# Optimization experiments

Measured on AMD Instinct MI355X. Metric: run time of the kernel, lower is better.

Reference implementation:

```python
import jax, jax.numpy as jnp
import numpy as np

KERNEL_SIZE = 16
STRIDE = 8
NEG = -1.0e9


def setup_inputs() -> dict:
    key = jax.random.key(0)
    k1, k2, k3, k4, k5 = jax.random.split(key, 5)
    B, C, L = 8, 512, 4096
    x = jax.random.normal(k1, (B, C, L), dtype=jnp.float32)
    mask = jax.random.randint(k2, (B, L), 0, 2).astype(bool)
    W = jax.random.normal(k3, (C, C), dtype=jnp.float32) * 0.02
    b = jax.random.normal(k4, (C,), dtype=jnp.float32) * 0.02
    v = jax.random.normal(k5, (C,), dtype=jnp.float32) * 0.02
    return {"x": x, "mask": mask, "W": W, "b": b, "v": v}


def reference(x, mask, W, b, v):
    # x: [B, C, L], mask: [B, L] (True = masked out)
    B, C, L = x.shape
    win, step = KERNEL_SIZE, STRIDE
    L_pool = 1 + (L - win) // step
    # per-token projection (identical across windows since proj is per-token)
    h = jnp.tanh(jnp.einsum('bcl,dc->bld', x, W) + b)      # [B, L, C]
    s = jnp.einsum('bld,d->bl', h, v)                       # [B, L]
    idx = jnp.arange(L_pool)[:, None] * step + jnp.arange(win)[None, :]
    sw = s[:, idx]
    mw = mask[:, idx]
    sw = jnp.where(mw, NEG, sw)
    w = jax.nn.softmax(sw, axis=-1)
    w = jnp.where(mw, 0.0, w)
    norm = jnp.clip(jnp.sum(w, axis=-1, keepdims=True), 1e-6, None)
    w = w / norm
    xw = x[:, :, idx]
    return jnp.einsum('bcpw,bpw->bcp', xw, w)               # [B, C, L_pool]
```

## Files before the change

kernel.cpp:

```cpp
#include <hip/hip_runtime.h>
#include <hip/hip_bf16.h>
#include <cmath>

#define Bsz 8
#define Csz 512
#define Lsz 4096
#define LPOOL 511
#define NEGV -1000000000.0f

typedef __attribute__((ext_vector_type(8))) short short8;
typedef __attribute__((ext_vector_type(4))) float float4v;

__device__ __forceinline__ float bf2f(short u) {
  unsigned int x = ((unsigned int)(unsigned short)u) << 16;
  return __builtin_bit_cast(float, x);
}

__device__ __forceinline__ float ftanh(float x) {
  float e = __expf(2.0f * x);
  return 1.0f - 2.0f * __builtin_amdgcn_rcpf(e + 1.0f);
}

__device__ __forceinline__ void gl_lds16(const __hip_bfloat16* g, void* l) {
  __builtin_amdgcn_global_load_lds(
      (const __attribute__((address_space(1))) unsigned int*)g,
      (__attribute__((address_space(3))) unsigned int*)l, 16, 0, 0);
}

__global__ __launch_bounds__(256) void prep(const unsigned char* __restrict__ mb,
    int* __restrict__ flag, const float* __restrict__ W,
    __hip_bfloat16* __restrict__ Wts) {
  const int tid = threadIdx.x;
  const int pb = blockIdx.x;
  if (pb == 0) {
    __shared__ int sf;
    if (tid == 0) sf = 0;
    __syncthreads();
    int f = 0;
    for (int i = tid; i < 4096; i += 256)
      if ((i & 3) && mb[i]) f = 1;
    if (f) atomicOr(&sf, 1);
    __syncthreads();
    if (tid == 0) *flag = sf;
  } else {
    int tg = (pb - 1) * 256 + tid;
    int d = tg >> 6, cg = tg & 63;
    float4 w0 = *(const float4*)(W + (size_t)d * 512 + cg * 8);
    float4 w1 = *(const float4*)(W + (size_t)d * 512 + cg * 8 + 4);
    __hip_bfloat16 hb[8];
    hb[0] = __float2bfloat16(w0.x); hb[1] = __float2bfloat16(w0.y);
    hb[2] = __float2bfloat16(w0.z); hb[3] = __float2bfloat16(w0.w);
    hb[4] = __float2bfloat16(w1.x); hb[5] = __float2bfloat16(w1.y);
    hb[6] = __float2bfloat16(w1.z); hb[7] = __float2bfloat16(w1.w);
    int nt = d >> 7, row = d & 127, ks = cg >> 2, seg = cg & 3;
    *(short8*)(Wts + (((size_t)nt * 16 + ks) * 512 + seg * 128 + row) * 8) = *(short8*)hb;
  }
}

__global__ __launch_bounds__(512, 2) void gemm_fused(
    const float* __restrict__ x, const __hip_bfloat16* __restrict__ Wts,
    const float* __restrict__ bias, const float* __restrict__ v,
    float* __restrict__ s, __hip_bfloat16* __restrict__ xbf) {
  __shared__ short8 sA[8192];
  __shared__ __align__(16) char sPool[17408];

  const int tid = threadIdx.x;
  const int lane = tid & 63, wave = tid >> 6;
  const int mt = blockIdx.x;
  const int b = mt >> 5;
  const int l0 = (mt & 31) << 7;

  {
    float* sXw = (float*)sPool + wave * 544;
    const int r = lane >> 1;
    const int q = lane & 1;
    const size_t rowbase =
        (((size_t)(b * Csz + r)) << 12) + (size_t)(l0 + wave * 16 + q * 8);
    const float* xg = x + rowbase;
    const int ll = lane & 15, kseg = lane >> 4;

    float4 a0 = *(const float4*)(xg);
    float4 a1 = *(const float4*)(xg + 4);
    float4 b0 = *(const float4*)(xg + (1u << 17));
    float4 b1 = *(const float4*)(xg + (1u << 17) + 4);
    float4 c0 = a0, c1 = a1;

    for (int cc = 0; cc < 16; ++cc) {
      if (cc < 14) {
        const float* xn = xg + ((size_t)(cc + 2) << 17);
        c0 = *(const float4*)(xn);
        c1 = *(const float4*)(xn + 4);
      }
      __hip_bfloat16 hb[8];
      hb[0] = __float2bfloat16(a0.x); hb[1] = __float2bfloat16(a0.y);
      hb[2] = __float2bfloat16(a0.z); hb[3] = __float2bfloat16(a0.w);
      hb[4] = __float2bfloat16(a1.x); hb[5] = __float2bfloat16(a1.y);
      hb[6] = __float2bfloat16(a1.z); hb[7] = __float2bfloat16(a1.w);
      *(short8*)(xbf + rowbase + ((size_t)cc << 17)) = *(short8*)hb;
      *(float4*)(&sXw[r * 17 + q * 8])     = a0;
      *(float4*)(&sXw[r * 17 + q * 8 + 4]) = a1;
      asm volatile("s_waitcnt lgkmcnt(0)" ::: "memory");
      __builtin_amdgcn_sched_barrier(0);
      float tv[8];
      #pragma unroll
      for (int j = 0; j < 8; ++j) tv[j] = sXw[(kseg * 8 + j) * 17 + ll];
      __hip_bfloat16 ab[8];
      #pragma unroll
      for (int j = 0; j < 8; ++j) ab[j] = __float2bfloat16(tv[j]);
      sA[(cc * 4 + kseg) * 128 + wave * 16 + ll] = *(short8*)ab;
      asm volatile("s_waitcnt lgkmcnt(0)" ::: "memory");
      __builtin_amdgcn_sched_barrier(0);
      a0 = b0; a1 = b1; b0 = c0; b1 = c1;
    }
  }

  const int lr = lane & 15, quad = lane >> 4;
  float bl[4][8], vl[4][8];
  #pragma unroll
  for (int nt = 0; nt < 4; ++nt)
    #pragma unroll
    for (int nf = 0; nf < 8; ++nf) {
      int n = nt * 128 + nf * 16 + lr;
      bl[nt][nf] = bias[n];
      vl[nt][nf] = v[n];
    }

  __syncthreads();
  short8 (*sB)[512] = (short8 (*)[512])sPool;
  gl_lds16(Wts + (size_t)(wave * 64 + lane) * 8, &sB[0][wave * 64]);
  __syncthreads();

  float4v acc[8];
  float sp[4];
  #pragma unroll
  for (int nf = 0; nf < 8; ++nf) acc[nf] = (float4v)0.f;
  #pragma unroll
  for (int reg = 0; reg < 4; ++reg) sp[reg] = 0.f;

  #pragma unroll
  for (int nt = 0; nt < 4; ++nt) {
    #pragma unroll 2
    for (int ks = 0; ks < 16; ++ks) {
      const int idx = nt * 16 + ks;
      const int cur = idx & 1;
      if (idx < 63) {
        const __hip_bfloat16* gb =
            Wts + ((size_t)(idx + 1) << 12) + (size_t)(wave * 64 + lane) * 8;
        gl_lds16(gb, &sB[cur ^ 1][wave * 64]);
        asm volatile("s_waitcnt vmcnt(1)" ::: "memory");
      } else {
        asm volatile("s_waitcnt vmcnt(0)" ::: "memory");
      }
      __builtin_amdgcn_sched_barrier(0);
      __builtin_amdgcn_s_barrier();
      short8 af = sA[(ks * 4 + quad) * 128 + wave * 16 + lr];
      short8 bfr[8];
      #pragma unroll
      for (int nf = 0; nf < 8; ++nf)
        bfr[nf] = sB[cur][quad * 128 + nf * 16 + lr];
      #pragma unroll
      for (int nf = 0; nf < 8; ++nf)
        acc[nf] = __builtin_amdgcn_mfma_f32_16x16x32_bf16(af, bfr[nf], acc[nf], 0, 0, 0);
      __builtin_amdgcn_s_barrier();
    }
    #pragma unroll
    for (int reg = 0; reg < 4; ++reg) {
      float pp = 0.f;
      #pragma unroll
      for (int nf = 0; nf < 8; ++nf)
        pp += ftanh(acc[nf][reg] + bl[nt][nf]) * vl[nt][nf];
      sp[reg] += pp;
    }
    #pragma unroll
    for (int nf = 0; nf < 8; ++nf) acc[nf] = (float4v)0.f;
  }

  #pragma unroll
  for (int reg = 0; reg < 4; ++reg) {
    float pv = sp[reg];
    pv += __shfl_xor(pv, 1, 16);
    pv += __shfl_xor(pv, 2, 16);
    pv += __shfl_xor(pv, 4, 16);
    pv += __shfl_xor(pv, 8, 16);
    if (lr == 0)
      s[mt * 128 + wave * 16 + quad * 4 + reg] = pv;
  }
}

__global__ __launch_bounds__(256) void pool2(const __hip_bfloat16* __restrict__ xbf,
    const float* __restrict__ s, const void* __restrict__ mask,
    const int* __restrict__ flag, float* __restrict__ out) {
  __shared__ float wl[8][17];
  const int t = threadIdx.x;
  const int p0 = blockIdx.x * 8, b = blockIdx.y;
  if (t < 8 && p0 + t < LPOOL) {
    const int p = p0 + t;
    const bool u8 = (*flag != 0);
    const unsigned char* m8 = (const unsigned char*)mask;
    const int* m32 = (const int*)mask;
    const int base = b * Lsz + p * 8;
    float sv[16]; int mv[16];
    float mx = -3.4e38f;
    #pragma unroll
    for (int w = 0; w < 16; ++w) {
      int mk = u8 ? (int)m8[base + w] : m32[base + w];
      float val = mk ? NEGV : s[base + w];
      sv[w] = val; mv[w] = mk;
      mx = fmaxf(mx, val);
    }
    float sum = 0.f;
    #pragma unroll
    for (int w = 0; w < 16; ++w) { sv[w] = expf(sv[w] - mx); sum += sv[w]; }
    float inv = 1.0f / sum;
    float norm = 0.f;
    #pragma unroll
    for (int w = 0; w < 16; ++w) { sv[w] = mv[w] ? 0.f : sv[w] * inv; norm += sv[w]; }
    norm = fmaxf(norm, 1e-6f);
    float rn = 1.0f / norm;
    #pragma unroll
    for (int w = 0; w < 16; ++w) wl[t][w] = sv[w] * rn;
  }
  __syncthreads();
  const int ci = t >> 3, pi = t & 7;
  const int p = p0 + pi;
  if (p >= LPOOL) return;
  float wr[16];
  #pragma unroll
  for (int w = 0; w < 16; ++w) wr[w] = wl[pi][w];
  #pragma unroll 4
  for (int it = 0; it < 16; ++it) {
    int c = it * 32 + ci;
    const __hip_bfloat16* xp = xbf + ((size_t)b * Csz + c) * Lsz + 8 * p;
    short8 lo = *(const short8*)xp;
    short8 hi = *(const short8*)(xp + 8);
    float acc = 0.f;
    #pragma unroll
    for (int j = 0; j < 8; ++j)
      acc += bf2f(lo[j]) * wr[j] + bf2f(hi[j]) * wr[8 + j];
    out[((size_t)b * Csz + c) * LPOOL + p] = acc;
  }
}

__global__ void detect_mask(const unsigned char* __restrict__ mb, int* __restrict__ flag) {
  __shared__ int sf;
  int t = threadIdx.x;
  if (t == 0) sf = 0;
  __syncthreads();
  int f = 0;
  for (int i = t; i < 4096; i += 256)
    if ((i & 3) && mb[i]) f = 1;
  if (f) atomicOr(&sf, 1);
  __syncthreads();
  if (t == 0) *flag = sf;
}

__global__ __launch_bounds__(256) void gemm_s_f32(const float* __restrict__ x,
    const float* __restrict__ W, const float* __restrict__ bias,
    const float* __restrict__ v, float* __restrict__ s_out) {
  __shared__ float sA[32][64];
  __shared__ float sB[32][68];
  __shared__ float s_acc[64];
  const int tid = threadIdx.x;
  const int b = blockIdx.y;
  const int l0 = blockIdx.x * 64;
  if (tid < 64) s_acc[tid] = 0.0f;
  const int tx = tid & 15;
  const int ty = tid >> 4;
  const float* xb = x + ((size_t)b * Csz) * Lsz + l0;
  for (int d0 = 0; d0 < Csz; d0 += 64) {
    float acc[4][4] = {{0.f}};
    for (int c0 = 0; c0 < Csz; c0 += 32) {
      __syncthreads();
      #pragma unroll
      for (int it = 0; it < 8; ++it) {
        int idx = tid + it * 256;
        int kc = idx >> 6, ml = idx & 63;
        sA[kc][ml] = xb[(size_t)(c0 + kc) * Lsz + ml];
      }
      #pragma unroll
      for (int it = 0; it < 8; ++it) {
        int idx = tid + it * 256;
        int kc = idx & 31, dj = idx >> 5;
        sB[kc][dj] = W[(size_t)(d0 + dj) * Csz + c0 + kc];
      }
      __syncthreads();
      #pragma unroll
      for (int kc = 0; kc < 32; ++kc) {
        float4 a  = *(const float4*)(&sA[kc][tx << 2]);
        float4 w4 = *(const float4*)(&sB[kc][ty << 2]);
        acc[0][0] += a.x * w4.x; acc[0][1] += a.x * w4.y; acc[0][2] += a.x * w4.z; acc[0][3] += a.x * w4.w;
        acc[1][0] += a.y * w4.x; acc[1][1] += a.y * w4.y; acc[1][2] += a.y * w4.z; acc[1][3] += a.y * w4.w;
        acc[2][0] += a.z * w4.x; acc[2][1] += a.z * w4.y; acc[2][2] += a.z * w4.z; acc[2][3] += a.z * w4.w;
        acc[3][0] += a.w * w4.x; acc[3][1] += a.w * w4.y; acc[3][2] += a.w * w4.z; acc[3][3] += a.w * w4.w;
      }
    }
    float part[4] = {0.f, 0.f, 0.f, 0.f};
    #pragma unroll
    for (int j = 0; j < 4; ++j) {
      int d = d0 + (ty << 2) + j;
      float bj = bias[d], vj = v[d];
      #pragma unroll
      for (int i = 0; i < 4; ++i)
        part[i] += tanhf(acc[i][j] + bj) * vj;
    }
    #pragma unroll
    for (int i = 0; i < 4; ++i)
      atomicAdd(&s_acc[(tx << 2) + i], part[i]);
  }
  __syncthreads();
  if (tid < 64) s_out[(size_t)b * Lsz + l0 + tid] = s_acc[tid];
}

__global__ void win_weights(const float* __restrict__ s, const void* __restrict__ mask,
                            const int* __restrict__ flag, float* __restrict__ wgt) {
  int t = blockIdx.x * blockDim.x + threadIdx.x;
  if (t >= Bsz * LPOOL) return;
  int b = t / LPOOL, p = t - b * LPOOL;
  const bool u8 = (*flag != 0);
  const unsigned char* m8 = (const unsigned char*)mask;
  const int* m32 = (const int*)mask;
  float sv[16]; int mv[16];
  float mx = -3.4e38f;
  int base = b * Lsz + p * 8;
  #pragma unroll
  for (int w = 0; w < 16; ++w) {
    int mk = u8 ? (int)m8[base + w] : m32[base + w];
    float val = mk ? NEGV : s[base + w];
    sv[w] = val; mv[w] = mk;
    mx = fmaxf(mx, val);
  }
  float sum = 0.f;
  #pragma unroll
  for (int w = 0; w < 16; ++w) { sv[w] = expf(sv[w] - mx); sum += sv[w]; }
  float inv = 1.0f / sum;
  float norm = 0.f;
  #pragma unroll
  for (int w = 0; w < 16; ++w) { sv[w] = mv[w] ? 0.f : sv[w] * inv; norm += sv[w]; }
  norm = fmaxf(norm, 1e-6f);
  float rn = 1.0f / norm;
  #pragma unroll
  for (int w = 0; w < 16; ++w) wgt[t * 16 + w] = sv[w] * rn;
}

__global__ __launch_bounds__(256) void pool_out(const float* __restrict__ x,
    const float* __restrict__ wgt, float* __restrict__ out) {
  __shared__ float xrow[Lsz];
  int bc = blockIdx.x;
  int c = bc & (Csz - 1);
  int b = bc >> 9;
  const float* xr = x + ((size_t)b * Csz + c) * Lsz;
  int tid = threadIdx.x;
  #pragma unroll
  for (int it = 0; it < 4; ++it) {
    int idx = (tid + it * 256) << 2;
    *(float4*)(&xrow[idx]) = *(const float4*)(&xr[idx]);
  }
  __syncthreads();
  const float* wb = wgt + (size_t)b * LPOOL * 16;
  float* ob = out + ((size_t)b * Csz + c) * LPOOL;
  for (int p = tid; p < LPOOL; p += 256) {
    const float4* wp = (const float4*)(wb + p * 16);
    const float4* xp = (const float4*)(&xrow[p * 8]);
    float acc = 0.f;
    #pragma unroll
    for (int q = 0; q < 4; ++q) {
      float4 wv = wp[q], xv = xp[q];
      acc += xv.x * wv.x + xv.y * wv.y + xv.z * wv.z + xv.w * wv.w;
    }
    ob[p] = acc;
  }
}

extern "C" void kernel_launch(void* const* d_in, const int* in_sizes, int n_in,
                              void* d_out, int out_size, void* d_ws, size_t ws_size,
                              hipStream_t stream) {
  const float* x    = (const float*)d_in[0];
  const void*  mask = d_in[1];
  const float* W    = (const float*)d_in[2];
  const float* bias = (const float*)d_in[3];
  const float* v    = (const float*)d_in[4];
  float* out = (float*)d_out;

  char* wsb = (char*)d_ws;
  int*   flag = (int*)wsb;
  float* s    = (float*)(wsb + 256);
  float* wgt  = (float*)(wsb + 131328);
  __hip_bfloat16* Wts = (__hip_bfloat16*)(wsb + 393216);
  __hip_bfloat16* xbf = (__hip_bfloat16*)(wsb + 917504);
  const size_t NEED = 917504 + 33554432;

  if (ws_size >= NEED) {
    prep<<<129, 256, 0, stream>>>((const unsigned char*)mask, flag, W, Wts);
    gemm_fused<<<256, 512, 0, stream>>>(x, Wts, bias, v, s, xbf);
    pool2<<<dim3(64, Bsz), 256, 0, stream>>>(xbf, s, mask, flag, out);
  } else {
    detect_mask<<<1, 256, 0, stream>>>((const unsigned char*)mask, flag);
    gemm_s_f32<<<dim3(Lsz / 64, Bsz), 256, 0, stream>>>(x, W, bias, v, s);
    win_weights<<<(Bsz * LPOOL + 255) / 256, 256, 0, stream>>>(s, mask, flag, wgt);
    pool_out<<<Bsz * Csz, 256, 0, stream>>>(x, wgt, out);
  }
}
```

Before: 163.9 us.

## Use single-wave GEMM blocks reading W directly from global, split pool over channels

```diff
diff --git a/kernel.cpp b/kernel.cpp
--- a/kernel.cpp
+++ b/kernel.cpp
@@ -19,12 +19,6 @@
 __device__ __forceinline__ float ftanh(float x) {
   float e = __expf(2.0f * x);
   return 1.0f - 2.0f * __builtin_amdgcn_rcpf(e + 1.0f);
-}
-
-__device__ __forceinline__ void gl_lds16(const __hip_bfloat16* g, void* l) {
-  __builtin_amdgcn_global_load_lds(
-      (const __attribute__((address_space(1))) unsigned int*)g,
-      (__attribute__((address_space(3))) unsigned int*)l, 16, 0, 0);
 }
 
 __global__ __launch_bounds__(256) void prep(const unsigned char* __restrict__ mb,
@@ -57,25 +51,24 @@
   }
 }
 
-__global__ __launch_bounds__(512, 2) void gemm_fused(
+__global__ __launch_bounds__(64, 2) void gemm_fused(
     const float* __restrict__ x, const __hip_bfloat16* __restrict__ Wts,
     const float* __restrict__ bias, const float* __restrict__ v,
     float* __restrict__ s, __hip_bfloat16* __restrict__ xbf) {
-  __shared__ short8 sA[8192];
-  __shared__ __align__(16) char sPool[17408];
-
-  const int tid = threadIdx.x;
-  const int lane = tid & 63, wave = tid >> 6;
+  __shared__ float sX[32][17];
+
+  const int lane = threadIdx.x;
   const int mt = blockIdx.x;
-  const int b = mt >> 5;
-  const int l0 = (mt & 31) << 7;
+  const int b = mt >> 8;
+  const int l0 = (mt & 255) << 4;
+
+  short8 af[16];
 
   {
-    float* sXw = (float*)sPool + wave * 544;
     const int r = lane >> 1;
     const int q = lane & 1;
     const size_t rowbase =
-        (((size_t)(b * Csz + r)) << 12) + (size_t)(l0 + wave * 16 + q * 8);
+        (((size_t)(b * Csz + r)) << 12) + (size_t)(l0 + q * 8);
     const float* xg = x + rowbase;
     const int ll = lane & 15, kseg = lane >> 4;
 
@@ -85,6 +78,7 @@
     float4 b1 = *(const float4*)(xg + (1u << 17) + 4);
     float4 c0 = a0, c1 = a1;
 
+    #pragma unroll
     for (int cc = 0; cc < 16; ++cc) {
       if (cc < 14) {
         const float* xn = xg + ((size_t)(cc + 2) << 17);
@@ -97,17 +91,17 @@
       hb[4] = __float2bfloat16(a1.x); hb[5] = __float2bfloat16(a1.y);
       hb[6] = __float2bfloat16(a1.z); hb[7] = __float2bfloat16(a1.w);
       *(short8*)(xbf + rowbase + ((size_t)cc << 17)) = *(short8*)hb;
-      *(float4*)(&sXw[r * 17 + q * 8])     = a0;
-      *(float4*)(&sXw[r * 17 + q * 8 + 4]) = a1;
+      *(float4*)(&sX[r][q * 8])     = a0;
+      *(float4*)(&sX[r][q * 8 + 4]) = a1;
       asm volatile("s_waitcnt lgkmcnt(0)" ::: "memory");
       __builtin_amdgcn_sched_barrier(0);
       float tv[8];
       #pragma unroll
-      for (int j = 0; j < 8; ++j) tv[j] = sXw[(kseg * 8 + j) * 17 + ll];
+      for (int j = 0; j < 8; ++j) tv[j] = sX[kseg * 8 + j][ll];
       __hip_bfloat16 ab[8];
       #pragma unroll
       for (int j = 0; j < 8; ++j) ab[j] = __float2bfloat16(tv[j]);
-      sA[(cc * 4 + kseg) * 128 + wave * 16 + ll] = *(short8*)ab;
+      af[cc] = *(short8*)ab;
       asm volatile("s_waitcnt lgkmcnt(0)" ::: "memory");
       __builtin_amdgcn_sched_barrier(0);
       a0 = b0; a1 = b1; b0 = c0; b1 = c1;
@@ -115,64 +109,41 @@
   }
 
   const int lr = lane & 15, quad = lane >> 4;
-  float bl[4][8], vl[4][8];
-  #pragma unroll
-  for (int nt = 0; nt < 4; ++nt)
+  float sp[4] = {0.f, 0.f, 0.f, 0.f};
+  const short8* Wt8 = (const short8*)Wts;
+
+  for (int nt = 0; nt < 4; ++nt) {
+    float bl[8], vl[8];
     #pragma unroll
     for (int nf = 0; nf < 8; ++nf) {
       int n = nt * 128 + nf * 16 + lr;
-      bl[nt][nf] = bias[n];
-      vl[nt][nf] = v[n];
-    }
-
-  __syncthreads();
-  short8 (*sB)[512] = (short8 (*)[512])sPool;
-  gl_lds16(Wts + (size_t)(wave * 64 + lane) * 8, &sB[0][wave * 64]);
-  __syncthreads();
-
-  float4v acc[8];
-  float sp[4];
-  #pragma unroll
-  for (int nf = 0; nf < 8; ++nf) acc[nf] = (float4v)0.f;
-  #pragma unroll
-  for (int reg = 0; reg < 4; ++reg) sp[reg] = 0.f;
-
-  #pragma unroll
-  for (int nt = 0; nt < 4; ++nt) {
-    #pragma unroll 2
+      bl[nf] = bias[n];
+      vl[nf] = v[n];
+    }
+    float4v acc[8];
+    #pragma unroll
+    for (int nf = 0; nf < 8; ++nf) acc[nf] = (float4v)0.f;
+
+    #pragma unroll
     for (int ks = 0; ks < 16; ++ks) {
-      const int idx = nt * 16 + ks;
-      const int cur = idx & 1;
-      if (idx < 63) {
-        const __hip_bfloat16* gb =
-            Wts + ((size_t)(idx + 1) << 12) + (size_t)(wave * 64 + lane) * 8;
-        gl_lds16(gb, &sB[cur ^ 1][wave * 64]);
-        asm volatile("s_waitcnt vmcnt(1)" ::: "memory");
-      } else {
-        asm volatile("s_waitcnt vmcnt(0)" ::: "memory");
-      }
-      __builtin_amdgcn_sched_barrier(0);
-      __builtin_amdgcn_s_barrier();
-      short8 af = sA[(ks * 4 + quad) * 128 + wave * 16 + lr];
+      const short8* bt = Wt8 + ((size_t)(nt * 16 + ks) * 512 + quad * 128 + lr);
       short8 bfr[8];
       #pragma unroll
+      for (int nf = 0; nf < 8; ++nf) bfr[nf] = bt[nf * 16];
+      #pragma unroll
       for (int nf = 0; nf < 8; ++nf)
-        bfr[nf] = sB[cur][quad * 128 + nf * 16 + lr];
-      #pragma unroll
-      for (int nf = 0; nf < 8; ++nf)
-        acc[nf] = __builtin_amdgcn_mfma_f32_16x16x32_bf16(af, bfr[nf], acc[nf], 0, 0, 0);
-      __builtin_amdgcn_s_barrier();
-    }
+        acc[nf] = __builtin_amdgcn_mfma_f32_16x16x32_bf16(
+            af[ks], bfr[nf], acc[nf], 0, 0, 0);
+    }
+
     #pragma unroll
     for (int reg = 0; reg < 4; ++reg) {
       float pp = 0.f;
       #pragma unroll
       for (int nf = 0; nf < 8; ++nf)
-        pp += ftanh(acc[nf][reg] + bl[nt][nf]) * vl[nt][nf];
+        pp += ftanh(acc[nf][reg] + bl[nf]) * vl[nf];
       sp[reg] += pp;
     }
-    #pragma unroll
-    for (int nf = 0; nf < 8; ++nf) acc[nf] = (float4v)0.f;
   }
 
   #pragma unroll
@@ -183,7 +154,7 @@
     pv += __shfl_xor(pv, 4, 16);
     pv += __shfl_xor(pv, 8, 16);
     if (lr == 0)
-      s[mt * 128 + wave * 16 + quad * 4 + reg] = pv;
+      s[mt * 16 + quad * 4 + reg] = pv;
   }
 }
 
@@ -193,6 +164,7 @@
   __shared__ float wl[8][17];
   const int t = threadIdx.x;
   const int p0 = blockIdx.x * 8, b = blockIdx.y;
+  const int ch = blockIdx.z;
   if (t < 8 && p0 + t < LPOOL) {
     const int p = p0 + t;
     const bool u8 = (*flag != 0);
@@ -227,9 +199,9 @@
   float wr[16];
   #pragma unroll
   for (int w = 0; w < 16; ++w) wr[w] = wl[pi][w];
-  #pragma unroll 4
-  for (int it = 0; it < 16; ++it) {
-    int c = it * 32 + ci;
+  #pragma unroll
+  for (int it = 0; it < 8; ++it) {
+    int c = ch * 256 + it * 32 + ci;
     const __hip_bfloat16* xp = xbf + ((size_t)b * Csz + c) * Lsz + 8 * p;
     short8 lo = *(const short8*)xp;
     short8 hi = *(const short8*)(xp + 8);
@@ -391,8 +363,8 @@
 
   if (ws_size >= NEED) {
     prep<<<129, 256, 0, stream>>>((const unsigned char*)mask, flag, W, Wts);
-    gemm_fused<<<256, 512, 0, stream>>>(x, Wts, bias, v, s, xbf);
-    pool2<<<dim3(64, Bsz), 256, 0, stream>>>(xbf, s, mask, flag, out);
+    gemm_fused<<<2048, 64, 0, stream>>>(x, Wts, bias, v, s, xbf);
+    pool2<<<dim3(64, Bsz, 2), 256, 0, stream>>>(xbf, s, mask, flag, out);
   } else {
     detect_mask<<<1, 256, 0, stream>>>((const unsigned char*)mask, flag);
     gemm_s_f32<<<dim3(Lsz / 64, Bsz), 256, 0, stream>>>(x, W, bias, v, s);
```

After: 266.4 us. 62.6% more time.

## Halve GEMM tile to 64 rows with 2x2 wave split and split pool channels

Applied to the files above, without the earlier changes.

```diff
diff --git a/kernel.cpp b/kernel.cpp
--- a/kernel.cpp
+++ b/kernel.cpp
@@ -57,18 +57,18 @@
   }
 }
 
-__global__ __launch_bounds__(512, 2) void gemm_fused(
+__global__ __launch_bounds__(256, 2) void gemm_fused(
     const float* __restrict__ x, const __hip_bfloat16* __restrict__ Wts,
     const float* __restrict__ bias, const float* __restrict__ v,
     float* __restrict__ s, __hip_bfloat16* __restrict__ xbf) {
-  __shared__ short8 sA[8192];
-  __shared__ __align__(16) char sPool[17408];
+  __shared__ short8 sA[4096];
+  __shared__ __align__(16) char sPool[16384];
 
   const int tid = threadIdx.x;
   const int lane = tid & 63, wave = tid >> 6;
   const int mt = blockIdx.x;
-  const int b = mt >> 5;
-  const int l0 = (mt & 31) << 7;
+  const int b = mt >> 6;
+  const int l0 = (mt & 63) << 6;
 
   {
     float* sXw = (float*)sPool + wave * 544;
@@ -107,7 +107,7 @@
       __hip_bfloat16 ab[8];
       #pragma unroll
       for (int j = 0; j < 8; ++j) ab[j] = __float2bfloat16(tv[j]);
-      sA[(cc * 4 + kseg) * 128 + wave * 16 + ll] = *(short8*)ab;
+      sA[(cc * 4 + kseg) * 64 + wave * 16 + ll] = *(short8*)ab;
       asm volatile("s_waitcnt lgkmcnt(0)" ::: "memory");
       __builtin_amdgcn_sched_barrier(0);
       a0 = b0; a1 = b1; b0 = c0; b1 = c1;
@@ -115,30 +115,41 @@
   }
 
   const int lr = lane & 15, quad = lane >> 4;
-  float bl[4][8], vl[4][8];
+  const int mh = wave >> 1, nh = wave & 1;
+
+  float bl[4][4], vl[4][4];
   #pragma unroll
   for (int nt = 0; nt < 4; ++nt)
     #pragma unroll
-    for (int nf = 0; nf < 8; ++nf) {
-      int n = nt * 128 + nf * 16 + lr;
+    for (int nf = 0; nf < 4; ++nf) {
+      int n = nt * 128 + nh * 64 + nf * 16 + lr;
       bl[nt][nf] = bias[n];
       vl[nt][nf] = v[n];
     }
 
   __syncthreads();
   short8 (*sB)[512] = (short8 (*)[512])sPool;
-  gl_lds16(Wts + (size_t)(wave * 64 + lane) * 8, &sB[0][wave * 64]);
-  __syncthreads();
-
-  float4v acc[8];
-  float sp[4];
-  #pragma unroll
-  for (int nf = 0; nf < 8; ++nf) acc[nf] = (float4v)0.f;
-  #pragma unroll
-  for (int reg = 0; reg < 4; ++reg) sp[reg] = 0.f;
+  {
+    const __hip_bfloat16* gb = Wts + (size_t)(wave * 64 + lane) * 8;
+    gl_lds16(gb,        &sB[0][wave * 64]);
+    gl_lds16(gb + 2048, &sB[0][256 + wave * 64]);
+  }
+  __syncthreads();
+
+  float sp[2][4];
+  #pragma unroll
+  for (int mf = 0; mf < 2; ++mf)
+    #pragma unroll
+    for (int reg = 0; reg < 4; ++reg) sp[mf][reg] = 0.f;
 
   #pragma unroll
   for (int nt = 0; nt < 4; ++nt) {
+    float4v acc[2][4];
+    #pragma unroll
+    for (int mf = 0; mf < 2; ++mf)
+      #pragma unroll
+      for (int nf = 0; nf < 4; ++nf) acc[mf][nf] = (float4v)0.f;
+
     #pragma unroll 2
     for (int ks = 0; ks < 16; ++ks) {
       const int idx = nt * 16 + ks;
@@ -146,44 +157,71 @@
       if (idx < 63) {
         const __hip_bfloat16* gb =
             Wts + ((size_t)(idx + 1) << 12) + (size_t)(wave * 64 + lane) * 8;
-        gl_lds16(gb, &sB[cur ^ 1][wave * 64]);
-        asm volatile("s_waitcnt vmcnt(1)" ::: "memory");
+        gl_lds16(gb,        &sB[cur ^ 1][wave * 64]);
+        gl_lds16(gb + 2048, &sB[cur ^ 1][256 + wave * 64]);
+        asm volatile("s_waitcnt vmcnt(2)" ::: "memory");
       } else {
         asm volatile("s_waitcnt vmcnt(0)" ::: "memory");
       }
       __builtin_amdgcn_sched_barrier(0);
       __builtin_amdgcn_s_barrier();
-      short8 af = sA[(ks * 4 + quad) * 128 + wave * 16 + lr];
-      short8 bfr[8];
-      #pragma unroll
-      for (int nf = 0; nf < 8; ++nf)
-        bfr[nf] = sB[cur][quad * 128 + nf * 16 + lr];
-      #pragma unroll
-      for (int nf = 0; nf < 8; ++nf)
-        acc[nf] = __builtin_amdgcn_mfma_f32_16x16x32_bf16(af, bfr[nf], acc[nf], 0, 0, 0);
+      short8 af[2], bfr[4];
+      #pragma unroll
+      for (int mf = 0; mf < 2; ++mf)
+        af[mf] = sA[(ks * 4 + quad) * 64 + mh * 32 + mf * 16 + lr];
+      #pragma unroll
+      for (int nf = 0; nf < 4; ++nf)
+        bfr[nf] = sB[cur][quad * 128 + nh * 64 + nf * 16 + lr];
+      __builtin_amdgcn_s_setprio(1);
+      #pragma unroll
+      for (int mf = 0; mf < 2; ++mf)
+        #pragma unroll
+        for (int nf = 0; nf < 4; ++nf)
+          acc[mf][nf] = __builtin_amdgcn_mfma_f32_16x16x32_bf16(
+              af[mf], bfr[nf], acc[mf][nf], 0, 0, 0);
+      __builtin_amdgcn_s_setprio(0);
       __builtin_amdgcn_s_barrier();
     }
     #pragma unroll
+    for (int mf = 0; mf < 2; ++mf)
+      #pragma unroll
+      for (int reg = 0; reg < 4; ++reg) {
+        float pp = 0.f;
+        #pragma unroll
+        for (int nf = 0; nf < 4; ++nf)
+          pp += ftanh(acc[mf][nf][reg] + bl[nt][nf]) * vl[nt][nf];
+        sp[mf][reg] += pp;
+      }
+  }
+
+  float* sRed = (float*)sPool;
+  float pv[2][4];
+  #pragma unroll
+  for (int mf = 0; mf < 2; ++mf)
+    #pragma unroll
     for (int reg = 0; reg < 4; ++reg) {
-      float pp = 0.f;
-      #pragma unroll
-      for (int nf = 0; nf < 8; ++nf)
-        pp += ftanh(acc[nf][reg] + bl[nt][nf]) * vl[nt][nf];
-      sp[reg] += pp;
-    }
-    #pragma unroll
-    for (int nf = 0; nf < 8; ++nf) acc[nf] = (float4v)0.f;
-  }
-
-  #pragma unroll
-  for (int reg = 0; reg < 4; ++reg) {
-    float pv = sp[reg];
-    pv += __shfl_xor(pv, 1, 16);
-    pv += __shfl_xor(pv, 2, 16);
-    pv += __shfl_xor(pv, 4, 16);
-    pv += __shfl_xor(pv, 8, 16);
-    if (lr == 0)
-      s[mt * 128 + wave * 16 + quad * 4 + reg] = pv;
+      float p = sp[mf][reg];
+      p += __shfl_xor(p, 1, 16);
+      p += __shfl_xor(p, 2, 16);
+      p += __shfl_xor(p, 4, 16);
+      p += __shfl_xor(p, 8, 16);
+      pv[mf][reg] = p;
+    }
+  if (nh == 1 && lr == 0) {
+    #pragma unroll
+    for (int mf = 0; mf < 2; ++mf)
+      #pragma unroll
+      for (int reg = 0; reg < 4; ++reg)
+        sRed[((mh * 2 + mf) * 4 + quad) * 4 + reg] = pv[mf][reg];
+  }
+  __syncthreads();
+  if (nh == 0 && lr == 0) {
+    #pragma unroll
+    for (int mf = 0; mf < 2; ++mf)
+      #pragma unroll
+      for (int reg = 0; reg < 4; ++reg)
+        s[mt * 64 + mh * 32 + mf * 16 + quad * 4 + reg] =
+            pv[mf][reg] + sRed[((mh * 2 + mf) * 4 + quad) * 4 + reg];
   }
 }
 
@@ -193,6 +231,7 @@
   __shared__ float wl[8][17];
   const int t = threadIdx.x;
   const int p0 = blockIdx.x * 8, b = blockIdx.y;
+  const int ch = blockIdx.z;
   if (t < 8 && p0 + t < LPOOL) {
     const int p = p0 + t;
     const bool u8 = (*flag != 0);
@@ -227,9 +266,9 @@
   float wr[16];
   #pragma unroll
   for (int w = 0; w < 16; ++w) wr[w] = wl[pi][w];
-  #pragma unroll 4
-  for (int it = 0; it < 16; ++it) {
-    int c = it * 32 + ci;
+  #pragma unroll
+  for (int it = 0; it < 8; ++it) {
+    int c = ch * 256 + it * 32 + ci;
     const __hip_bfloat16* xp = xbf + ((size_t)b * Csz + c) * Lsz + 8 * p;
     short8 lo = *(const short8*)xp;
     short8 hi = *(const short8*)(xp + 8);
@@ -391,8 +430,8 @@
 
   if (ws_size >= NEED) {
     prep<<<129, 256, 0, stream>>>((const unsigned char*)mask, flag, W, Wts);
-    gemm_fused<<<256, 512, 0, stream>>>(x, Wts, bias, v, s, xbf);
-    pool2<<<dim3(64, Bsz), 256, 0, stream>>>(xbf, s, mask, flag, out);
+    gemm_fused<<<512, 256, 0, stream>>>(x, Wts, bias, v, s, xbf);
+    pool2<<<dim3(64, Bsz, 2), 256, 0, stream>>>(xbf, s, mask, flag, out);
   } else {
     detect_mask<<<1, 256, 0, stream>>>((const unsigned char*)mask, flag);
     gemm_s_f32<<<dim3(Lsz / 64, Bsz), 256, 0, stream>>>(x, W, bias, v, s);
```

Result: faster. 159.7 us (-2.5%).
